# Performance work log

Measured on AMD Instinct MI355X. Metric: run time of the kernel, lower is better.

## Reference

```python
import jax, jax.numpy as jnp
import numpy as np

B, L, D, M_MAX = 4, 4096, 1024, 512


def setup_inputs() -> dict:
    key = jax.random.key(0)
    k_ct, k_enc, k_lo, k_hi, k_w = jax.random.split(key, 5)
    concept_tokens = jax.random.normal(k_ct, (B, M_MAX, D), dtype=jnp.float32)
    encoder_out = jax.random.normal(k_enc, (B, L, D), dtype=jnp.float32)
    # sorted unique boundary positions per batch, first boundary at position 0
    rng = np.random.RandomState(0)
    idx = np.stack([np.sort(rng.choice(np.arange(1, L), size=M_MAX - 1, replace=False)) for _ in range(B)])
    boundary_idx = jnp.asarray(np.concatenate([np.zeros((B, 1), dtype=np.int64), idx], axis=1))  # [B, M_max]
    # probs < 0.5 everywhere except at boundary positions (>= 0.5), so cumsum(mask)-1 < M_max
    lo = jax.random.uniform(k_lo, (B, L), minval=0.02, maxval=0.48)
    hi = jax.random.uniform(k_hi, (B, M_MAX), minval=0.5, maxval=1.0)
    rows = jnp.arange(B)[:, None]
    boundary_probs = lo.at[rows, boundary_idx].set(hi)
    concept_mask = jnp.ones((B, M_MAX), dtype=bool)
    W = jax.random.normal(k_w, (D, D), dtype=jnp.float32) * 0.02  # residual_proj.weight (out = x @ W.T)
    return {"concept_tokens": concept_tokens, "encoder_out": encoder_out,
            "boundary_probs": boundary_probs, "boundary_idx": boundary_idx,
            "concept_mask": concept_mask, "W": W}


def _ema_smooth(concept_tokens, p_at_bounds):
    """h_i = (1-p_i)*h_{i-1} + p_i*c_i via associative scan; h_0 = c_0."""
    h0 = concept_tokens[:, 0]                                  # [B, d]
    p_rest = p_at_bounds[:, 1:]                                # [B, M-1]
    decay = jnp.clip(1.0 - p_rest, 1e-7, None)
    b = p_rest[..., None] * concept_tokens[:, 1:]              # [B, M-1, d]
    a = jnp.broadcast_to(decay[..., None], b.shape)

    def combine(x, y):
        a1, b1 = x
        a2, b2 = y
        return a1 * a2, a2 * b1 + b2

    A, Bc = jax.lax.associative_scan(combine, (a, b), axis=1)
    h_rest = A * h0[:, None, :] + Bc                           # h_i = A_i*h0 + B_i
    return jnp.concatenate([h0[:, None, :], h_rest], axis=1)   # [B, M, d]


def reference(concept_tokens, encoder_out, boundary_probs, boundary_idx, concept_mask, W):
    d = encoder_out.shape[-1]
    # Eq.5: EMA over concept tokens with boundary probs gathered at boundary positions
    p_raw = jnp.take_along_axis(boundary_probs, boundary_idx, axis=1)          # [B, M]
    p_at_bounds = jnp.where(concept_mask, p_raw, 1.0)
    p_at_bounds = jnp.clip(p_at_bounds, 0.1, None)
    smoothed = _ema_smooth(concept_tokens, p_at_bounds)                        # [B, M, d]
    # Eq.8: plug-back via running boundary count
    boundary_mask = boundary_probs >= 0.5                                      # [B, L]
    plug_back_idx = jnp.clip(jnp.cumsum(boundary_mask.astype(jnp.int32), axis=1) - 1, 0, None)
    plugback = jnp.take_along_axis(smoothed, plug_back_idx[..., None], axis=1)  # [B, L, d]
    # Eq.6/7/9: confidence + STE (forward value is exactly 1.0)
    b_f = boundary_mask.astype(boundary_probs.dtype)
    c_t = b_f * boundary_probs + (1.0 - b_f) * (1.0 - boundary_probs)
    ste_c = c_t + jax.lax.stop_gradient(1.0 - c_t)
    upsampled = ste_c[..., None] * plugback
    # Eq.3: residual linear (no bias)
    return upsampled + jnp.einsum('bld,ed->ble', encoder_out, W)
```

## Files before the change

kernel.cpp:

```cpp
#include <hip/hip_runtime.h>
#include <hip/hip_bf16.h>
#include <stdint.h>


#define B_  4
#define L_  4096
#define D_  1024
#define M_  512

typedef __attribute__((ext_vector_type(8))) short bf16x8;
typedef __attribute__((ext_vector_type(4))) float f32x4;
typedef __attribute__((ext_vector_type(8))) unsigned short u16x8;

__device__ inline unsigned short f2bf(float f) {
    unsigned u = __float_as_uint(f);
    u += 0x7fffu + ((u >> 16) & 1u);
    return (unsigned short)(u >> 16);
}

__global__ void prep_all_kernel(const float* __restrict__ enc, const float* __restrict__ W,
                                const float* __restrict__ probs, const float* __restrict__ ct,
                                const int* __restrict__ bidx,
                                unsigned short* __restrict__ encb, unsigned short* __restrict__ Wb,
                                int* __restrict__ pbi, float* __restrict__ smoothed,
                                int encBlocks) {
    __shared__ int part[512];
    __shared__ float ad[M_], bdp[M_];
    __shared__ float Ac[8][64], Bc[8][64], Hin[8][64];

    const int blk = blockIdx.x;
    const int t   = threadIdx.x;

    if (blk < encBlocks + 256) {
        const float* src; unsigned short* dst; size_t i;
        if (blk < encBlocks) { src = enc; dst = encb; i = (size_t)blk * 512 + t; }
        else                 { src = W;   dst = Wb;   i = (size_t)(blk - encBlocks) * 512 + t; }
        float4 x0 = ((const float4*)src)[2 * i];
        float4 x1 = ((const float4*)src)[2 * i + 1];
        u16x8 v;
        v[0] = f2bf(x0.x); v[1] = f2bf(x0.y); v[2] = f2bf(x0.z); v[3] = f2bf(x0.w);
        v[4] = f2bf(x1.x); v[5] = f2bf(x1.y); v[6] = f2bf(x1.z); v[7] = f2bf(x1.w);
        ((u16x8*)dst)[i] = v;
    } else if (blk < encBlocks + 260) {
        int b = blk - (encBlocks + 256);
        const float4* pr = (const float4*)(probs + b * L_);
        int cnt[8]; int s = 0;
        #pragma unroll
        for (int u = 0; u < 2; ++u) {
            float4 x = pr[t * 2 + u];
            s += (x.x >= 0.5f); cnt[u * 4 + 0] = s;
            s += (x.y >= 0.5f); cnt[u * 4 + 1] = s;
            s += (x.z >= 0.5f); cnt[u * 4 + 2] = s;
            s += (x.w >= 0.5f); cnt[u * 4 + 3] = s;
        }
        part[t] = s;
        __syncthreads();
        for (int off = 1; off < 512; off <<= 1) {
            int x = part[t];
            int y = (t >= off) ? part[t - off] : 0;
            __syncthreads();
            part[t] = x + y;
            __syncthreads();
        }
        int excl = part[t] - s;
        int4* po = (int4*)(pbi + b * L_ + t * 8);
        #pragma unroll
        for (int u = 0; u < 2; ++u) {
            int4 o;
            o.x = max(excl + cnt[u * 4 + 0] - 1, 0);
            o.y = max(excl + cnt[u * 4 + 1] - 1, 0);
            o.z = max(excl + cnt[u * 4 + 2] - 1, 0);
            o.w = max(excl + cnt[u * 4 + 3] - 1, 0);
            po[u] = o;
        }
    } else {
        int idx = blk - (encBlocks + 260);
        int b  = idx >> 4;
        int d0 = (idx & 15) * 64;
        int dl = t & 63;
        int ch = t >> 6;
        {
            int m = t;
            int bi = bidx[b * M_ + m];
            float p = fmaxf(probs[b * L_ + bi], 0.1f);
            ad[m]  = (m == 0) ? 0.0f : fmaxf(1.0f - p, 1e-7f);
            bdp[m] = (m == 0) ? 1.0f : p;
        }
        __syncthreads();
        const float* ctp = ct + ((size_t)b * M_ + ch * 64) * D_ + d0 + dl;
        float A = 1.0f, Bv = 0.0f;
        #pragma unroll 8
        for (int i = 0; i < 64; ++i) {
            int m = ch * 64 + i;
            float c = ctp[(size_t)i * D_];
            A  = ad[m] * A;
            Bv = ad[m] * Bv + bdp[m] * c;
        }
        Ac[ch][dl] = A; Bc[ch][dl] = Bv;
        __syncthreads();
        if (t < 64) {
            float H = 0.0f;
            #pragma unroll
            for (int c = 0; c < 8; ++c) {
                Hin[c][t] = H;
                H = Ac[c][t] * H + Bc[c][t];
            }
        }
        __syncthreads();
        float h = Hin[ch][dl];
        float* smp = smoothed + ((size_t)b * M_ + ch * 64) * D_ + d0 + dl;
        #pragma unroll 8
        for (int i = 0; i < 64; ++i) {
            int m = ch * 64 + i;
            float c = ctp[(size_t)i * D_];
            h = ad[m] * h + bdp[m] * c;
            smp[(size_t)i * D_] = h;
        }
    }
}

#define NTT 16

__global__ __launch_bounds__(512, 2) void gemm8_kernel(
    const unsigned short* __restrict__ encb, const unsigned short* __restrict__ Wb,
    const float* __restrict__ smoothed, const int* __restrict__ pbi,
    float* __restrict__ out)
{
    __shared__ __align__(16) char smem[131072];

    const int tid  = threadIdx.x;
    const int lane = tid & 63;
    const int w    = tid >> 6;
    const int wm   = w >> 2;
    const int wn   = w & 3;
    const int l15  = lane & 15;
    const int l16  = lane >> 4;

    const int orig = blockIdx.x;
    const int rm   = (orig & 7) * 32 + (orig >> 3);
    const size_t rowBase = (size_t)(rm >> 2) * 256;
    const int    colBase = (rm & 3) * 256;

    const int rsw   = (l15 & 7) << 4;
    const int colb0 = (0  + l16 * 16) ^ rsw;
    const int colb1 = (64 + l16 * 16) ^ rsw;

    const int aRd0 = (0 + wm) * 16384 + l15 * 128;
    const int aRd1 = (2 + wm) * 16384 + l15 * 128;
    const int bRd0 = 65536 + (0 + (wn >> 1)) * 16384 + ((wn & 1) * 64 + l15) * 128;
    const int bRd1 = 65536 + (2 + (wn >> 1)) * 16384 + ((wn & 1) * 64 + l15) * 128;

    const int srow  = tid >> 3;
    const int sslot = (tid & 7) ^ ((tid >> 3) & 7);
    const unsigned short* aSrc = encb + (rowBase + srow) * D_ + sslot * 8;
    const unsigned short* bSrc = Wb + ((size_t)colBase + srow) * D_ + sslot * 8;

#define STAGE_A(T, db, h)                                                                 \
  { _Pragma("unroll") for (int i_ = 0; i_ < 2; ++i_) {                                    \
      const unsigned short* g_ = aSrc + (size_t)((h) * 128 + i_ * 64) * D_ + (T) * 64;    \
      __builtin_amdgcn_global_load_lds(                                                   \
          (const __attribute__((address_space(1))) void*)g_,                              \
          (__attribute__((address_space(3))) void*)(smem + ((db)*2+(h))*16384 + i_*8192 + tid*16), \
          16, 0, 0); } }

#define STAGE_B(T, db, h)                                                                 \
  { _Pragma("unroll") for (int i_ = 0; i_ < 2; ++i_) {                                    \
      const unsigned short* g_ = bSrc + (size_t)((h) * 128 + i_ * 64) * D_ + (T) * 64;    \
      __builtin_amdgcn_global_load_lds(                                                   \
          (const __attribute__((address_space(1))) void*)g_,                              \
          (__attribute__((address_space(3))) void*)(smem + 65536 + ((db)*2+(h))*16384 + i_*8192 + tid*16), \
          16, 0, 0); } }

#define LDSA(aRd, mbase)                                                                  \
  { _Pragma("unroll") for (int m_ = 0; m_ < 4; ++m_) {                                    \
      a[m_*2+0] = *(const bf16x8*)(smem + (aRd) + ((mbase)+m_)*2048 + colb0);             \
      a[m_*2+1] = *(const bf16x8*)(smem + (aRd) + ((mbase)+m_)*2048 + colb1); } }

#define LDSB(bRd, nbase)                                                                  \
  { _Pragma("unroll") for (int n_ = 0; n_ < 2; ++n_) {                                    \
      b[((nbase)+n_)*2+0] = *(const bf16x8*)(smem + (bRd) + ((nbase)+n_)*2048 + colb0);   \
      b[((nbase)+n_)*2+1] = *(const bf16x8*)(smem + (bRd) + ((nbase)+n_)*2048 + colb1); } }

#define MFMA_Q(mbase, nbase)                                                              \
  { _Pragma("unroll") for (int m_ = 0; m_ < 4; ++m_)                                      \
    _Pragma("unroll") for (int n_ = 0; n_ < 2; ++n_) {                                    \
      acc[(mbase)+m_][(nbase)+n_] = __builtin_amdgcn_mfma_f32_16x16x32_bf16(              \
          a[m_*2+0], b[((nbase)+n_)*2+0], acc[(mbase)+m_][(nbase)+n_], 0, 0, 0);          \
      acc[(mbase)+m_][(nbase)+n_] = __builtin_amdgcn_mfma_f32_16x16x32_bf16(              \
          a[m_*2+1], b[((nbase)+n_)*2+1], acc[(mbase)+m_][(nbase)+n_], 0, 0, 0); } }

#define PH_OPEN()  do { __builtin_amdgcn_sched_barrier(0); __builtin_amdgcn_s_barrier();  \
    __builtin_amdgcn_sched_barrier(0);                                                    \
    asm volatile("s_waitcnt lgkmcnt(0)" ::: "memory");                                    \
    __builtin_amdgcn_sched_barrier(0); __builtin_amdgcn_s_setprio(1); } while (0)

#define PH_CLOSE() do { __builtin_amdgcn_s_setprio(0); __builtin_amdgcn_sched_barrier(0); \
    __builtin_amdgcn_s_barrier(); __builtin_amdgcn_sched_barrier(0); } while (0)

    f32x4 acc[8][4] = {};
    bf16x8 a[8], b[8];

    STAGE_A(0, 0, 0); STAGE_A(0, 0, 1);
    STAGE_B(0, 0, 0); STAGE_B(0, 0, 1);
    STAGE_B(1, 1, 0); STAGE_B(1, 1, 1);
    asm volatile("s_waitcnt vmcnt(4)" ::: "memory");
    __builtin_amdgcn_s_barrier();
    __builtin_amdgcn_sched_barrier(0);

    #pragma unroll 1
    for (int i = 0; i < NTT / 2; ++i) {
        const int t1 = 2 * i + 1;
        const int t2 = (2 * i + 2 < NTT) ? 2 * i + 2 : NTT - 1;
        const int t3 = (2 * i + 3 < NTT) ? 2 * i + 3 : NTT - 1;
        LDSA(aRd0, 0); LDSB(bRd0, 0);
        STAGE_A(t1, 1, 0);
        PH_OPEN(); MFMA_Q(0, 0); PH_CLOSE();
        LDSB(bRd0, 2);
        STAGE_A(t1, 1, 1);
        PH_OPEN(); MFMA_Q(0, 2); PH_CLOSE();
        LDSA(aRd0, 4);
        STAGE_B(t2, 0, 0);
        PH_OPEN(); MFMA_Q(4, 0); PH_CLOSE();
        STAGE_B(t2, 0, 1);
        asm volatile("s_waitcnt vmcnt(4)" ::: "memory");
        PH_OPEN(); MFMA_Q(4, 2); PH_CLOSE();
        LDSA(aRd1, 0); LDSB(bRd1, 0);
        STAGE_A(t2, 0, 0);
        PH_OPEN(); MFMA_Q(0, 0); PH_CLOSE();
        LDSB(bRd1, 2);
        STAGE_A(t2, 0, 1);
        PH_OPEN(); MFMA_Q(0, 2); PH_CLOSE();
        LDSA(aRd1, 4);
        STAGE_B(t3, 1, 0);
        PH_OPEN(); MFMA_Q(4, 0); PH_CLOSE();
        STAGE_B(t3, 1, 1);
        asm volatile("s_waitcnt vmcnt(4)" ::: "memory");
        PH_OPEN(); MFMA_Q(4, 2); PH_CLOSE();
    }
#undef STAGE_A
#undef STAGE_B
#undef LDSA
#undef LDSB
#undef MFMA_Q
#undef PH_OPEN
#undef PH_CLOSE

    #pragma unroll
    for (int m = 0; m < 8; ++m) {
        const size_t row0 = rowBase + wm * 128 + m * 16;
        #pragma unroll
        for (int j = 0; j < 4; ++j) {
            size_t row = row0 + l16 * 4 + j;
            int bb2 = (int)(row >> 12);
            int pb  = pbi[row];
            pb = pb < (M_ - 1) ? pb : (M_ - 1);
            const float* sm = smoothed + ((size_t)(bb2 * M_ + pb)) * D_;
            #pragma unroll
            for (int n = 0; n < 4; ++n) {
                int col = colBase + wn * 64 + n * 16 + l15;
                out[row * D_ + col] = acc[m][n][j] + sm[col];
            }
        }
    }
}

#define LDP 72
__global__ __launch_bounds__(256, 2) void gemm_fused_kernel(
    const float* __restrict__ enc, const unsigned short* __restrict__ Wb,
    const float* __restrict__ smoothed, const int* __restrict__ pbi,
    float* __restrict__ out)
{
    __shared__ unsigned short Asf[128][LDP];
    __shared__ unsigned short Bsf[128][LDP];
    const int tid  = threadIdx.x;
    const int lane = tid & 63;
    const int wid  = tid >> 6;
    const int wm   = wid >> 1;
    const int wn   = wid & 1;
    const int l15  = lane & 15;
    const int l16  = lane >> 4;
    const size_t rowBase = (size_t)blockIdx.x * 128;
    const int    colBase = blockIdx.y * 128;
    f32x4 acc[4][4] = {};
    for (int t = 0; t < D_ / 64; ++t) {
        const int k0 = t * 64;
        #pragma unroll
        for (int i = 0; i < 4; ++i) {
            int c = i * 256 + tid;
            int r = c >> 3;
            int c8 = c & 7;
            const float4* g = (const float4*)(enc + (rowBase + r) * D_ + k0 + c8 * 8);
            float4 x0 = g[0];
            float4 x1 = g[1];
            u16x8 v;
            v[0] = f2bf(x0.x); v[1] = f2bf(x0.y); v[2] = f2bf(x0.z); v[3] = f2bf(x0.w);
            v[4] = f2bf(x1.x); v[5] = f2bf(x1.y); v[6] = f2bf(x1.z); v[7] = f2bf(x1.w);
            *(u16x8*)&Asf[r][c8 * 8] = v;
        }
        #pragma unroll
        for (int i = 0; i < 4; ++i) {
            int c = i * 256 + tid;
            int r = c >> 3;
            int c8 = c & 7;
            u16x8 v = *(const u16x8*)(Wb + (size_t)(colBase + r) * D_ + k0 + c8 * 8);
            *(u16x8*)&Bsf[r][c8 * 8] = v;
        }
        __syncthreads();
        #pragma unroll
        for (int kk = 0; kk < 2; ++kk) {
            bf16x8 a[4], bbf[4];
            #pragma unroll
            for (int m = 0; m < 4; ++m)
                a[m] = *(const bf16x8*)&Asf[wm * 64 + m * 16 + l15][kk * 32 + l16 * 8];
            #pragma unroll
            for (int n = 0; n < 4; ++n)
                bbf[n] = *(const bf16x8*)&Bsf[wn * 64 + n * 16 + l15][kk * 32 + l16 * 8];
            #pragma unroll
            for (int m = 0; m < 4; ++m)
                #pragma unroll
                for (int n = 0; n < 4; ++n)
                    acc[m][n] = __builtin_amdgcn_mfma_f32_16x16x32_bf16(a[m], bbf[n], acc[m][n], 0, 0, 0);
        }
        __syncthreads();
    }
    #pragma unroll
    for (int m = 0; m < 4; ++m) {
        #pragma unroll
        for (int j = 0; j < 4; ++j) {
            size_t row = rowBase + wm * 64 + m * 16 + l16 * 4 + j;
            int b  = (int)(row >> 12);
            int pb = pbi[row];
            pb = pb < (M_ - 1) ? pb : (M_ - 1);
            const float* sm = smoothed + ((size_t)(b * M_ + pb)) * D_;
            #pragma unroll
            for (int n = 0; n < 4; ++n) {
                int col = colBase + wn * 64 + n * 16 + l15;
                out[row * D_ + col] = acc[m][n][j] + sm[col];
            }
        }
    }
}

extern "C" void kernel_launch(void* const* d_in, const int* in_sizes, int n_in,
                              void* d_out, int out_size, void* d_ws, size_t ws_size,
                              hipStream_t stream) {
    const float* ct    = (const float*)d_in[0];
    const float* enc   = (const float*)d_in[1];
    const float* probs = (const float*)d_in[2];
    const int*   bidx  = (const int*)d_in[3];
    const float* W     = (const float*)d_in[5];
    float* out = (float*)d_out;
    char*  ws  = (char*)d_ws;

    const size_t SZ_ENCB = (size_t)B_ * L_ * D_ * 2;
    const size_t SZ_SM   = (size_t)B_ * M_ * D_ * 4;
    const size_t SZ_PBI  = (size_t)B_ * L_ * 4;
    const size_t SZ_WB   = (size_t)D_ * D_ * 2;

    if (ws_size >= SZ_ENCB + SZ_SM + SZ_PBI + SZ_WB) {
        unsigned short* encb     = (unsigned short*)ws;
        float*          smoothed = (float*)(ws + SZ_ENCB);
        int*            pbi      = (int*)(ws + SZ_ENCB + SZ_SM);
        unsigned short* Wb       = (unsigned short*)(ws + SZ_ENCB + SZ_SM + SZ_PBI);

        const int encBlocks = B_ * L_ * D_ / 4096;
        const int nBlocks   = encBlocks + 256 + B_ + B_ * D_ / 64;
        hipLaunchKernelGGL(prep_all_kernel, dim3(nBlocks), dim3(512), 0, stream,
                           enc, W, probs, ct, bidx, encb, Wb, pbi, smoothed, encBlocks);
        hipLaunchKernelGGL(gemm8_kernel, dim3(256), dim3(512), 0, stream,
                           encb, Wb, smoothed, pbi, out);
    } else {
        float*          smoothed = (float*)ws;
        int*            pbi      = (int*)(ws + SZ_SM);
        unsigned short* Wb       = (unsigned short*)(ws + SZ_SM + SZ_PBI);
        const int nBlocks = 0 + 256 + B_ + B_ * D_ / 64;
        hipLaunchKernelGGL(prep_all_kernel, dim3(nBlocks), dim3(512), 0, stream,
                           enc, W, probs, ct, bidx, (unsigned short*)ws , Wb, pbi, smoothed, 0);
        hipLaunchKernelGGL(gemm_fused_kernel, dim3(B_ * L_ / 128, D_ / 128), dim3(256), 0, stream,
                           enc, Wb, smoothed, pbi, out);
    }
}
```

Baseline: 171.8 us.

## Fuse fp32-to-bf16 conversion of encoder_out into GEMM A-tile staging

The separate prep pass that converted the full encoder_out tensor to bf16 in workspace is removed. The main GEMM now loads fp32 A tiles into registers, converts them to bf16, and writes them to swizzled LDS itself, prefetching one k-tile ahead. This avoids writing and then re-reading a 32MB bf16 copy. In exchange the A path moves from async global_load_lds to register-staged loads, which raises register pressure and puts conversion ALU work inside the MFMA loop.

```diff
diff --git a/kernel.cpp b/kernel.cpp
--- a/kernel.cpp
+++ b/kernel.cpp
@@ -18,12 +18,11 @@
     return (unsigned short)(u >> 16);
 }
 
-__global__ void prep_all_kernel(const float* __restrict__ enc, const float* __restrict__ W,
-                                const float* __restrict__ probs, const float* __restrict__ ct,
-                                const int* __restrict__ bidx,
-                                unsigned short* __restrict__ encb, unsigned short* __restrict__ Wb,
-                                int* __restrict__ pbi, float* __restrict__ smoothed,
-                                int encBlocks) {
+__global__ void prep_lite_kernel(const float* __restrict__ W,
+                                 const float* __restrict__ probs, const float* __restrict__ ct,
+                                 const int* __restrict__ bidx,
+                                 unsigned short* __restrict__ Wb,
+                                 int* __restrict__ pbi, float* __restrict__ smoothed) {
     __shared__ int part[512];
     __shared__ float ad[M_], bdp[M_];
     __shared__ float Ac[8][64], Bc[8][64], Hin[8][64];
@@ -31,18 +30,16 @@
     const int blk = blockIdx.x;
     const int t   = threadIdx.x;
 
-    if (blk < encBlocks + 256) {
-        const float* src; unsigned short* dst; size_t i;
-        if (blk < encBlocks) { src = enc; dst = encb; i = (size_t)blk * 512 + t; }
-        else                 { src = W;   dst = Wb;   i = (size_t)(blk - encBlocks) * 512 + t; }
-        float4 x0 = ((const float4*)src)[2 * i];
-        float4 x1 = ((const float4*)src)[2 * i + 1];
+    if (blk < 256) {
+        size_t i = (size_t)blk * 512 + t;
+        float4 x0 = ((const float4*)W)[2 * i];
+        float4 x1 = ((const float4*)W)[2 * i + 1];
         u16x8 v;
         v[0] = f2bf(x0.x); v[1] = f2bf(x0.y); v[2] = f2bf(x0.z); v[3] = f2bf(x0.w);
         v[4] = f2bf(x1.x); v[5] = f2bf(x1.y); v[6] = f2bf(x1.z); v[7] = f2bf(x1.w);
-        ((u16x8*)dst)[i] = v;
-    } else if (blk < encBlocks + 260) {
-        int b = blk - (encBlocks + 256);
+        ((u16x8*)Wb)[i] = v;
+    } else if (blk < 260) {
+        int b = blk - 256;
         const float4* pr = (const float4*)(probs + b * L_);
         int cnt[8]; int s = 0;
         #pragma unroll
@@ -74,7 +71,7 @@
             po[u] = o;
         }
     } else {
-        int idx = blk - (encBlocks + 260);
+        int idx = blk - 260;
         int b  = idx >> 4;
         int d0 = (idx & 15) * 64;
         int dl = t & 63;
@@ -122,7 +119,7 @@
 #define NTT 16
 
 __global__ __launch_bounds__(512, 2) void gemm8_kernel(
-    const unsigned short* __restrict__ encb, const unsigned short* __restrict__ Wb,
+    const float* __restrict__ enc, const unsigned short* __restrict__ Wb,
     const float* __restrict__ smoothed, const int* __restrict__ pbi,
     float* __restrict__ out)
 {
@@ -150,18 +147,37 @@
     const int bRd0 = 65536 + (0 + (wn >> 1)) * 16384 + ((wn & 1) * 64 + l15) * 128;
     const int bRd1 = 65536 + (2 + (wn >> 1)) * 16384 + ((wn & 1) * 64 + l15) * 128;
 
+    const int arow = tid >> 2;
+    const int as0  = (tid & 3) * 2;
+    const int asrc0 = ((as0    ) ^ (arow & 7)) * 8;
+    const int asrc1 = ((as0 + 1) ^ (arow & 7)) * 8;
+    const float* encA = enc + (rowBase + arow) * D_;
+    const int awr0 = arow * 128 + as0 * 16;
+    const int awr1 = arow * 128 + as0 * 16 + 16;
+
     const int srow  = tid >> 3;
     const int sslot = (tid & 7) ^ ((tid >> 3) & 7);
-    const unsigned short* aSrc = encb + (rowBase + srow) * D_ + sslot * 8;
     const unsigned short* bSrc = Wb + ((size_t)colBase + srow) * D_ + sslot * 8;
 
-#define STAGE_A(T, db, h)                                                                 \
-  { _Pragma("unroll") for (int i_ = 0; i_ < 2; ++i_) {                                    \
-      const unsigned short* g_ = aSrc + (size_t)((h) * 128 + i_ * 64) * D_ + (T) * 64;    \
-      __builtin_amdgcn_global_load_lds(                                                   \
-          (const __attribute__((address_space(1))) void*)g_,                              \
-          (__attribute__((address_space(3))) void*)(smem + ((db)*2+(h))*16384 + i_*8192 + tid*16), \
-          16, 0, 0); } }
+#define ISSUE_A(T, h, R, bank)                                                            \
+  { const float* s_ = encA + (size_t)(h) * 128 * D_ + (T) * 64;                           \
+    R[(bank)*4+0] = *(const float4*)(s_ + asrc0);                                         \
+    R[(bank)*4+1] = *(const float4*)(s_ + asrc0 + 4);                                     \
+    R[(bank)*4+2] = *(const float4*)(s_ + asrc1);                                         \
+    R[(bank)*4+3] = *(const float4*)(s_ + asrc1 + 4); }
+
+#define WRITE_A(db, h, R, bank)                                                           \
+  { u16x8 w0, w1;                                                                         \
+    w0[0]=f2bf(R[(bank)*4+0].x); w0[1]=f2bf(R[(bank)*4+0].y);                             \
+    w0[2]=f2bf(R[(bank)*4+0].z); w0[3]=f2bf(R[(bank)*4+0].w);                             \
+    w0[4]=f2bf(R[(bank)*4+1].x); w0[5]=f2bf(R[(bank)*4+1].y);                             \
+    w0[6]=f2bf(R[(bank)*4+1].z); w0[7]=f2bf(R[(bank)*4+1].w);                             \
+    w1[0]=f2bf(R[(bank)*4+2].x); w1[1]=f2bf(R[(bank)*4+2].y);                             \
+    w1[2]=f2bf(R[(bank)*4+2].z); w1[3]=f2bf(R[(bank)*4+2].w);                             \
+    w1[4]=f2bf(R[(bank)*4+3].x); w1[5]=f2bf(R[(bank)*4+3].y);                             \
+    w1[6]=f2bf(R[(bank)*4+3].z); w1[7]=f2bf(R[(bank)*4+3].w);                             \
+    *(u16x8*)(smem + ((db)*2+(h))*16384 + awr0) = w0;                                     \
+    *(u16x8*)(smem + ((db)*2+(h))*16384 + awr1) = w1; }
 
 #define STAGE_B(T, db, h)                                                                 \
   { _Pragma("unroll") for (int i_ = 0; i_ < 2; ++i_) {                                    \
@@ -199,45 +215,51 @@
 
     f32x4 acc[8][4] = {};
     bf16x8 a[8], b[8];
-
-    STAGE_A(0, 0, 0); STAGE_A(0, 0, 1);
+    float4 ra[8], rb[8];
+
+    ISSUE_A(0, 0, ra, 0); ISSUE_A(0, 1, ra, 1);
+    ISSUE_A(1, 0, rb, 0); ISSUE_A(1, 1, rb, 1);
     STAGE_B(0, 0, 0); STAGE_B(0, 0, 1);
     STAGE_B(1, 1, 0); STAGE_B(1, 1, 1);
-    asm volatile("s_waitcnt vmcnt(4)" ::: "memory");
+    WRITE_A(0, 0, ra, 0); WRITE_A(0, 1, ra, 1);
+    WRITE_A(1, 0, rb, 0); WRITE_A(1, 1, rb, 1);
+    asm volatile("s_waitcnt vmcnt(0) lgkmcnt(0)" ::: "memory");
     __builtin_amdgcn_s_barrier();
     __builtin_amdgcn_sched_barrier(0);
 
     #pragma unroll 1
     for (int i = 0; i < NTT / 2; ++i) {
-        const int t1 = 2 * i + 1;
         const int t2 = (2 * i + 2 < NTT) ? 2 * i + 2 : NTT - 1;
         const int t3 = (2 * i + 3 < NTT) ? 2 * i + 3 : NTT - 1;
         LDSA(aRd0, 0); LDSB(bRd0, 0);
-        STAGE_A(t1, 1, 0);
+        ISSUE_A(t2, 0, ra, 0);
         PH_OPEN(); MFMA_Q(0, 0); PH_CLOSE();
         LDSB(bRd0, 2);
-        STAGE_A(t1, 1, 1);
+        ISSUE_A(t2, 1, ra, 1);
         PH_OPEN(); MFMA_Q(0, 2); PH_CLOSE();
         LDSA(aRd0, 4);
         STAGE_B(t2, 0, 0);
         PH_OPEN(); MFMA_Q(4, 0); PH_CLOSE();
         STAGE_B(t2, 0, 1);
-        asm volatile("s_waitcnt vmcnt(4)" ::: "memory");
+        asm volatile("s_waitcnt vmcnt(2)" ::: "memory");
+        WRITE_A(0, 0, ra, 0); WRITE_A(0, 1, ra, 1);
         PH_OPEN(); MFMA_Q(4, 2); PH_CLOSE();
         LDSA(aRd1, 0); LDSB(bRd1, 0);
-        STAGE_A(t2, 0, 0);
+        ISSUE_A(t3, 0, ra, 0);
         PH_OPEN(); MFMA_Q(0, 0); PH_CLOSE();
         LDSB(bRd1, 2);
-        STAGE_A(t2, 0, 1);
+        ISSUE_A(t3, 1, ra, 1);
         PH_OPEN(); MFMA_Q(0, 2); PH_CLOSE();
         LDSA(aRd1, 4);
         STAGE_B(t3, 1, 0);
         PH_OPEN(); MFMA_Q(4, 0); PH_CLOSE();
         STAGE_B(t3, 1, 1);
-        asm volatile("s_waitcnt vmcnt(4)" ::: "memory");
+        asm volatile("s_waitcnt vmcnt(2)" ::: "memory");
+        WRITE_A(1, 0, ra, 0); WRITE_A(1, 1, ra, 1);
         PH_OPEN(); MFMA_Q(4, 2); PH_CLOSE();
     }
-#undef STAGE_A
+#undef ISSUE_A
+#undef WRITE_A
 #undef STAGE_B
 #undef LDSA
 #undef LDSB
@@ -264,83 +286,6 @@
     }
 }
 
-#define LDP 72
-__global__ __launch_bounds__(256, 2) void gemm_fused_kernel(
-    const float* __restrict__ enc, const unsigned short* __restrict__ Wb,
-    const float* __restrict__ smoothed, const int* __restrict__ pbi,
-    float* __restrict__ out)
-{
-    __shared__ unsigned short Asf[128][LDP];
-    __shared__ unsigned short Bsf[128][LDP];
-    const int tid  = threadIdx.x;
-    const int lane = tid & 63;
-    const int wid  = tid >> 6;
-    const int wm   = wid >> 1;
-    const int wn   = wid & 1;
-    const int l15  = lane & 15;
-    const int l16  = lane >> 4;
-    const size_t rowBase = (size_t)blockIdx.x * 128;
-    const int    colBase = blockIdx.y * 128;
-    f32x4 acc[4][4] = {};
-    for (int t = 0; t < D_ / 64; ++t) {
-        const int k0 = t * 64;
-        #pragma unroll
-        for (int i = 0; i < 4; ++i) {
-            int c = i * 256 + tid;
-            int r = c >> 3;
-            int c8 = c & 7;
-            const float4* g = (const float4*)(enc + (rowBase + r) * D_ + k0 + c8 * 8);
-            float4 x0 = g[0];
-            float4 x1 = g[1];
-            u16x8 v;
-            v[0] = f2bf(x0.x); v[1] = f2bf(x0.y); v[2] = f2bf(x0.z); v[3] = f2bf(x0.w);
-            v[4] = f2bf(x1.x); v[5] = f2bf(x1.y); v[6] = f2bf(x1.z); v[7] = f2bf(x1.w);
-            *(u16x8*)&Asf[r][c8 * 8] = v;
-        }
-        #pragma unroll
-        for (int i = 0; i < 4; ++i) {
-            int c = i * 256 + tid;
-            int r = c >> 3;
-            int c8 = c & 7;
-            u16x8 v = *(const u16x8*)(Wb + (size_t)(colBase + r) * D_ + k0 + c8 * 8);
-            *(u16x8*)&Bsf[r][c8 * 8] = v;
-        }
-        __syncthreads();
-        #pragma unroll
-        for (int kk = 0; kk < 2; ++kk) {
-            bf16x8 a[4], bbf[4];
-            #pragma unroll
-            for (int m = 0; m < 4; ++m)
-                a[m] = *(const bf16x8*)&Asf[wm * 64 + m * 16 + l15][kk * 32 + l16 * 8];
-            #pragma unroll
-            for (int n = 0; n < 4; ++n)
-                bbf[n] = *(const bf16x8*)&Bsf[wn * 64 + n * 16 + l15][kk * 32 + l16 * 8];
-            #pragma unroll
-            for (int m = 0; m < 4; ++m)
-                #pragma unroll
-                for (int n = 0; n < 4; ++n)
-                    acc[m][n] = __builtin_amdgcn_mfma_f32_16x16x32_bf16(a[m], bbf[n], acc[m][n], 0, 0, 0);
-        }
-        __syncthreads();
-    }
-    #pragma unroll
-    for (int m = 0; m < 4; ++m) {
-        #pragma unroll
-        for (int j = 0; j < 4; ++j) {
-            size_t row = rowBase + wm * 64 + m * 16 + l16 * 4 + j;
-            int b  = (int)(row >> 12);
-            int pb = pbi[row];
-            pb = pb < (M_ - 1) ? pb : (M_ - 1);
-            const float* sm = smoothed + ((size_t)(b * M_ + pb)) * D_;
-            #pragma unroll
-            for (int n = 0; n < 4; ++n) {
-                int col = colBase + wn * 64 + n * 16 + l15;
-                out[row * D_ + col] = acc[m][n][j] + sm[col];
-            }
-        }
-    }
-}
-
 extern "C" void kernel_launch(void* const* d_in, const int* in_sizes, int n_in,
                               void* d_out, int out_size, void* d_ws, size_t ws_size,
                               hipStream_t stream) {
@@ -352,31 +297,14 @@
     float* out = (float*)d_out;
     char*  ws  = (char*)d_ws;
 
-    const size_t SZ_ENCB = (size_t)B_ * L_ * D_ * 2;
-    const size_t SZ_SM   = (size_t)B_ * M_ * D_ * 4;
-    const size_t SZ_PBI  = (size_t)B_ * L_ * 4;
-    const size_t SZ_WB   = (size_t)D_ * D_ * 2;
-
-    if (ws_size >= SZ_ENCB + SZ_SM + SZ_PBI + SZ_WB) {
-        unsigned short* encb     = (unsigned short*)ws;
-        float*          smoothed = (float*)(ws + SZ_ENCB);
-        int*            pbi      = (int*)(ws + SZ_ENCB + SZ_SM);
-        unsigned short* Wb       = (unsigned short*)(ws + SZ_ENCB + SZ_SM + SZ_PBI);
-
-        const int encBlocks = B_ * L_ * D_ / 4096;
-        const int nBlocks   = encBlocks + 256 + B_ + B_ * D_ / 64;
-        hipLaunchKernelGGL(prep_all_kernel, dim3(nBlocks), dim3(512), 0, stream,
-                           enc, W, probs, ct, bidx, encb, Wb, pbi, smoothed, encBlocks);
-        hipLaunchKernelGGL(gemm8_kernel, dim3(256), dim3(512), 0, stream,
-                           encb, Wb, smoothed, pbi, out);
-    } else {
-        float*          smoothed = (float*)ws;
-        int*            pbi      = (int*)(ws + SZ_SM);
-        unsigned short* Wb       = (unsigned short*)(ws + SZ_SM + SZ_PBI);
-        const int nBlocks = 0 + 256 + B_ + B_ * D_ / 64;
-        hipLaunchKernelGGL(prep_all_kernel, dim3(nBlocks), dim3(512), 0, stream,
-                           enc, W, probs, ct, bidx, (unsigned short*)ws , Wb, pbi, smoothed, 0);
-        hipLaunchKernelGGL(gemm_fused_kernel, dim3(B_ * L_ / 128, D_ / 128), dim3(256), 0, stream,
-                           enc, Wb, smoothed, pbi, out);
-    }
+    const size_t SZ_SM  = (size_t)B_ * M_ * D_ * 4;
+    const size_t SZ_PBI = (size_t)B_ * L_ * 4;
+    float*          smoothed = (float*)ws;
+    int*            pbi      = (int*)(ws + SZ_SM);
+    unsigned short* Wb       = (unsigned short*)(ws + SZ_SM + SZ_PBI);
+
+    hipLaunchKernelGGL(prep_lite_kernel, dim3(324), dim3(512), 0, stream,
+                       W, probs, ct, bidx, Wb, pbi, smoothed);
+    hipLaunchKernelGGL(gemm8_kernel, dim3(256), dim3(512), 0, stream,
+                       enc, Wb, smoothed, pbi, out);
 }
```

New measurement: 203.7 us. +18.6%, slower.
